# Performance work log

Measured on AMD Instinct MI355X. Metric: run time of the kernel, lower is better.

Reference implementation:

```python
import jax, jax.numpy as jnp
import numpy as np

L, H, NH, F, S_MAX, VOCAB, STAR_V, OFF = 12, 768, 12, 3072, 512, 31090, 390, 30700
EPS = 1e-12

def _ln(x, g, b):
    m = x.mean(-1, keepdims=True)
    v = ((x - m) ** 2).mean(-1, keepdims=True)
    return (x - m) * jax.lax.rsqrt(v + EPS) * g + b

def setup_inputs() -> dict:
    key = jax.random.key(0)
    ks = iter(jax.random.split(key, 48))
    B, S = 16, 512
    p = lambda *s: jax.random.normal(next(ks), s, dtype=jnp.float32) * 0.02
    return dict(
        input_ids=jax.random.randint(next(ks), (B, S), 0, VOCAB),
        attention_mask=jnp.ones((B, S), dtype=jnp.int32),
        token_type_ids=jnp.zeros((B, S), dtype=jnp.int32),
        word_emb=p(VOCAB, H), star_emb=p(STAR_V, H),
        pos_emb=p(S_MAX, H), type_emb=p(2, H),
        emb_g=jnp.ones(H), emb_b=jnp.zeros(H),
        Wq=p(L, H, H), bq=jnp.zeros((L, H)), Wk=p(L, H, H), bk=jnp.zeros((L, H)),
        Wv=p(L, H, H), bv=jnp.zeros((L, H)), Wo=p(L, H, H), bo=jnp.zeros((L, H)),
        g1=jnp.ones((L, H)), b1=jnp.zeros((L, H)),
        Wi=p(L, H, F), bi=jnp.zeros((L, F)), Wf=p(L, F, H), bf=jnp.zeros((L, H)),
        g2=jnp.ones((L, H)), b2=jnp.zeros((L, H)),
        pool_W=p(H, H), pool_b=jnp.zeros(H))

def reference(input_ids, attention_mask, token_type_ids, word_emb, star_emb,
              pos_emb, type_emb, emb_g, emb_b, Wq, bq, Wk, bk, Wv, bv, Wo, bo,
              g1, b1, Wi, bi, Wf, bf, g2, b2, pool_W, pool_b):
    B, S = input_ids.shape
    dh = H // NH
    # vectorized masked embedding swap (replaces the per-token Python loop)
    star = input_ids >= OFF
    embs = jnp.where(star[..., None],
                     star_emb[jnp.clip(input_ids - OFF, 0, STAR_V - 1)],
                     word_emb[jnp.clip(input_ids, 0, VOCAB - 1)])
    x = _ln(embs + pos_emb[:S][None] + type_emb[token_type_ids], emb_g, emb_b)
    ext = (1.0 - attention_mask.astype(x.dtype))[:, None, None, :] * -10000.0
    scale = 1.0 / np.sqrt(dh).astype(np.float32)

    def layer(x, pr):
        wq, bq_, wk, bk_, wv, bv_, wo, bo_, g1_, b1_, wi, bi_, wf, bf_, g2_, b2_ = pr
        sp = lambda t: t.reshape(B, S, NH, dh).transpose(0, 2, 1, 3)  # [B,NH,S,dh]
        q, k, v = sp(x @ wq + bq_), sp(x @ wk + bk_), sp(x @ wv + bv_)
        att = jax.nn.softmax(jnp.einsum('bhqd,bhkd->bhqk', q, k) * scale + ext, axis=-1)
        ctx = jnp.einsum('bhqk,bhkd->bhqd', att, v).transpose(0, 2, 1, 3).reshape(B, S, H)
        x = _ln(x + ctx @ wo + bo_, g1_, b1_)
        x = _ln(x + jax.nn.gelu(x @ wi + bi_, approximate=False) @ wf + bf_, g2_, b2_)
        return x, None

    x, _ = jax.lax.scan(layer, x, (Wq, bq, Wk, bk, Wv, bv, Wo, bo,
                                   g1, b1, Wi, bi, Wf, bf, g2, b2))
    pooled = jnp.tanh(x[:, 0] @ pool_W + pool_b)
    return x, pooled
```

## Files before the change

### kernel.cpp

```cpp
#include <hip/hip_runtime.h>
#include <hip/hip_bf16.h>
#include <math.h>


#define L_   12
#define H_   768
#define NH_  12
#define DH_  64
#define F_   3072
#define B_   16
#define S_   512
#define NTOK (B_ * S_)
#define QKVN 2304

typedef __attribute__((ext_vector_type(8))) __bf16 bf16x8;
typedef __attribute__((ext_vector_type(4))) __bf16 bf16x4;
typedef __attribute__((ext_vector_type(4))) float  f32x4;

static __device__ __forceinline__ f32x4 mfma16(bf16x8 a, bf16x8 b, f32x4 c) {
  return __builtin_amdgcn_mfma_f32_16x16x32_bf16(a, b, c, 0, 0, 0);
}

static __device__ __forceinline__ void load_lds16(const void* g, void* l) {
  __builtin_amdgcn_global_load_lds(
      (const __attribute__((address_space(1))) void*)g,
      (__attribute__((address_space(3))) void*)l, 16, 0, 0);
}

static __device__ __forceinline__ float gelu_fast(float v) {
  const float u = 1.5957691216057308f * v * (1.0f + 0.044715f * v * v);
  return v / (1.0f + __expf(-u));
}

__global__ __launch_bounds__(256) void transpose_k(const float* __restrict__ in,
                                                   __bf16* __restrict__ out,
                                                   int R, int C, size_t outZ) {
  __shared__ float t[32][33];
  const int z = blockIdx.z;
  const float* inz = in + (size_t)z * R * C;
  __bf16* outz = out + (size_t)z * outZ;
  const int c0 = blockIdx.x * 32, r0 = blockIdx.y * 32;
  const int tx = threadIdx.x, ty = threadIdx.y;
#pragma unroll
  for (int i = 0; i < 32; i += 8)
    t[ty + i][tx] = inz[(size_t)(r0 + ty + i) * C + c0 + tx];
  __syncthreads();
#pragma unroll
  for (int i = 0; i < 32; i += 8)
    outz[(size_t)(c0 + ty + i) * R + r0 + tx] = (__bf16)t[tx][ty + i];
}

__global__ __launch_bounds__(256) void concat_bias(const float* __restrict__ bq,
                                                   const float* __restrict__ bk,
                                                   const float* __restrict__ bv,
                                                   float* __restrict__ o) {
  const int i = blockIdx.x * 256 + threadIdx.x;
  if (i >= L_ * QKVN) return;
  const int l = i / QKVN, j = i - l * QKVN;
  float v;
  if (j < H_) v = bq[l * H_ + j];
  else if (j < 2 * H_) v = bk[l * H_ + j - H_];
  else v = bv[l * H_ + j - 2 * H_];
  o[i] = v;
}

template <int EPI, int OUTBF, int VT>
__global__ __launch_bounds__(256, 3) void gemm_n64(const __bf16* __restrict__ A,
                                                   const __bf16* __restrict__ Bt,
                                                   const float* __restrict__ bias,
                                                   float* __restrict__ Cf,
                                                   __bf16* __restrict__ Cb,
                                                   __bf16* __restrict__ vtp,
                                                   int M, int N, int K, int Ntiles) {
  alignas(16) __shared__ __bf16 lds[24576];
  const int tid = threadIdx.x, wid = tid >> 6, lane = tid & 63;
  int bid = blockIdx.x;
  const int nwg = gridDim.x;
  if ((nwg & 7) == 0) bid = (bid & 7) * (nwg >> 3) + (bid >> 3);
  const int bm = (bid / Ntiles) << 7, bn = (bid % Ntiles) << 6;
  const int nt = K >> 6;

  const __bf16* pA[4];
  const __bf16* pB[2];
#pragma unroll
  for (int j = 0; j < 4; ++j) {
    const int E = (j << 11) + tid * 8;
    const int Ep = E ^ (((E >> 8) & 1) << 4);
    const int r = ((Ep >> 10) << 4) | ((Ep >> 5) & 15);
    const int c = (((Ep >> 9) & 1) << 5) | (Ep & 31);
    pA[j] = A + (size_t)(bm + r) * K + c;
    if (j < 2) pB[j] = Bt + (size_t)(bn + r) * K + c;
  }

  auto stage = [&](int t, int buf) {
    __bf16* base = &lds[buf * 12288 + (wid << 9)];
    const size_t off = (size_t)(t << 6);
#pragma unroll
    for (int j = 0; j < 4; ++j) load_lds16(pA[j] + off, base + (j << 11));
#pragma unroll
    for (int j = 0; j < 2; ++j) load_lds16(pB[j] + off, base + 8192 + (j << 11));
  };

  const int frow = lane & 15, fk = (lane >> 4) << 3;
  const int swzb = (frow * 32 + fk) ^ (((frow >> 3) & 1) << 4);
  const int mh = wid >> 1, nq = wid & 1;

  f32x4 acc[4][2] = {};

  stage(0, 0);
  asm volatile("s_waitcnt vmcnt(0)" ::: "memory");
  __builtin_amdgcn_s_barrier();

  for (int t = 0; t < nt; ++t) {
    const int buf = t & 1;
    if (t + 1 < nt) stage(t + 1, buf ^ 1);
    const __bf16* LA = &lds[buf * 12288 + (mh << 12)];
    const __bf16* LB = &lds[buf * 12288 + 8192 + (nq << 11)];
    bf16x8 a[4][2], b[2][2];
#pragma unroll
    for (int mi = 0; mi < 4; ++mi)
#pragma unroll
      for (int ks = 0; ks < 2; ++ks)
        a[mi][ks] = *(const bf16x8*)&LA[mi * 1024 + ks * 512 + swzb];
#pragma unroll
    for (int ni = 0; ni < 2; ++ni)
#pragma unroll
      for (int ks = 0; ks < 2; ++ks)
        b[ni][ks] = *(const bf16x8*)&LB[ni * 1024 + ks * 512 + swzb];
    asm volatile("s_waitcnt lgkmcnt(0)" ::: "memory");
    __builtin_amdgcn_s_setprio(1);
#pragma unroll
    for (int mi = 0; mi < 4; ++mi)
#pragma unroll
      for (int ni = 0; ni < 2; ++ni)
#pragma unroll
        for (int ks = 0; ks < 2; ++ks)
          acc[mi][ni] = mfma16(a[mi][ks], b[ni][ks], acc[mi][ni]);
    __builtin_amdgcn_s_setprio(0);
    asm volatile("s_waitcnt vmcnt(0)" ::: "memory");
    __builtin_amdgcn_s_barrier();
  }

  const int r0 = (lane >> 4) << 2, c0 = lane & 15;
  const int wrow = bm + (mh << 6), wcol = bn + (nq << 5);
#pragma unroll
  for (int ni = 0; ni < 2; ++ni) {
    const int col = wcol + (ni << 4) + c0;
    const float bv = bias[col];
    if (VT && (wcol + (ni << 4)) >= 2 * H_) {
      const int hh = (col - 2 * H_) >> 6, dd = (col - 2 * H_) & 63;
#pragma unroll
      for (int mi = 0; mi < 4; ++mi) {
        const int row = wrow + (mi << 4) + r0;
        bf16x4 pv;
#pragma unroll
        for (int r = 0; r < 4; ++r) pv[r] = (__bf16)(acc[mi][ni][r] + bv);
        const int bb2 = row >> 9, ss = row & 511;
        *(bf16x4*)&vtp[((size_t)(bb2 * NH_ + hh) * DH_ + dd) * S_ + ss] = pv;
      }
    } else {
#pragma unroll
      for (int mi = 0; mi < 4; ++mi) {
        const int row = wrow + (mi << 4) + r0;
#pragma unroll
        for (int r = 0; r < 4; ++r) {
          float v = acc[mi][ni][r] + bv;
          if (EPI == 1) v = gelu_fast(v);
          if (OUTBF)
            Cb[(size_t)(row + r) * N + col] = (__bf16)v;
          else
            Cf[(size_t)(row + r) * N + col] = v;
        }
      }
    }
  }
}

__global__ __launch_bounds__(256, 3) void attn_kernel(const __bf16* __restrict__ qkv,
                                                      const __bf16* __restrict__ vt,
                                                      const int* __restrict__ amask,
                                                      __bf16* __restrict__ ctx) {
  __shared__ float extm[S_];
  alignas(16) __shared__ __bf16 Kl[2][2048];
  alignas(16) __shared__ __bf16 Vl[2][2048];
  __shared__ __bf16 Pl[4][2][16][40];
  const int h = blockIdx.x, b = blockIdx.y, z = blockIdx.z;
  const int tid = threadIdx.x, wid = tid >> 6, lane = tid & 63;
  const size_t rowb = (size_t)b * S_ * QKVN + (size_t)h * DH_;
  const __bf16* vbase = vt + ((size_t)(b * NH_ + h) * DH_) * S_;

  for (int i = tid; i < S_; i += 256)
    extm[i] = (1.0f - (float)amask[b * S_ + i]) * -10000.0f;

  const int E = tid * 8;
  const int Ep = E ^ (((E >> 8) & 1) << 4);
  const int krow = ((Ep >> 10) << 4) | ((Ep >> 5) & 15);
  const int kcol = (((Ep >> 9) & 1) << 5) | (Ep & 31);
  const __bf16* ksrc = qkv + rowb + (size_t)krow * QKVN + H_ + kcol;
  const int vd = ((Ep >> 9) << 4) | ((Ep >> 5) & 15);
  const int vs = Ep & 31;
  const __bf16* vsrc = vbase + (size_t)vd * S_ + vs;

  auto stageKV = [&](int kt, int buf) {
    load_lds16(ksrc + (size_t)(kt * 32) * QKVN, &Kl[buf][E]);
    load_lds16(vsrc + kt * 32, &Vl[buf][E]);
  };

  const int c0 = lane & 15, g4 = lane >> 4;
  const int swzb = (c0 * 32 + (g4 << 3)) ^ (((c0 >> 3) & 1) << 4);
  const int qt0 = z * 8 + wid * 2;
  bf16x8 qf[2][2];
#pragma unroll
  for (int qi = 0; qi < 2; ++qi) {
    const __bf16* qrow = qkv + rowb +
        (size_t)((qt0 + qi) * 16 + c0) * QKVN + (g4 << 3);
    qf[qi][0] = *(const bf16x8*)qrow;
    qf[qi][1] = *(const bf16x8*)(qrow + 32);
  }
  f32x4 oacc[2][4] = {};
  float mrow[2] = {-1e30f, -1e30f}, lsum[2] = {0.f, 0.f};

  stageKV(0, 0);
  asm volatile("s_waitcnt vmcnt(0)" ::: "memory");
  __syncthreads();

#pragma unroll
  for (int kt = 0; kt < 16; ++kt) {
    const int buf = kt & 1;
    if (kt + 1 < 16) stageKV(kt + 1, buf ^ 1);
    bf16x8 kf[2][2], vf[4];
#pragma unroll
    for (int f = 0; f < 2; ++f)
#pragma unroll
      for (int half = 0; half < 2; ++half)
        kf[f][half] = *(const bf16x8*)&Kl[buf][f * 1024 + half * 512 + swzb];
#pragma unroll
    for (int dt = 0; dt < 4; ++dt)
      vf[dt] = *(const bf16x8*)&Vl[buf][dt * 512 + swzb];
    asm volatile("s_waitcnt lgkmcnt(0)" ::: "memory");
#pragma unroll
    for (int qi = 0; qi < 2; ++qi) {
      f32x4 sc[2];
      __builtin_amdgcn_s_setprio(1);
#pragma unroll
      for (int f = 0; f < 2; ++f) {
        f32x4 z2 = {};
        z2 = mfma16(kf[f][0], qf[qi][0], z2);
        z2 = mfma16(kf[f][1], qf[qi][1], z2);
#pragma unroll
        for (int r = 0; r < 4; ++r)
          sc[f][r] = z2[r] * 0.125f + extm[kt * 32 + f * 16 + (g4 << 2) + r];
      }
      __builtin_amdgcn_s_setprio(0);
      float mx = fmaxf(fmaxf(fmaxf(sc[0][0], sc[0][1]), fmaxf(sc[0][2], sc[0][3])),
                       fmaxf(fmaxf(sc[1][0], sc[1][1]), fmaxf(sc[1][2], sc[1][3])));
      mx = fmaxf(mx, __shfl_xor(mx, 16, 64));
      mx = fmaxf(mx, __shfl_xor(mx, 32, 64));
      const float mn = fmaxf(mrow[qi], mx);
      const float al = __expf(mrow[qi] - mn);
      mrow[qi] = mn;
      float rs = 0.f;
      bf16x4 p0, p1;
#pragma unroll
      for (int r = 0; r < 4; ++r) {
        const float pa0 = __expf(sc[0][r] - mn);
        const float pa1 = __expf(sc[1][r] - mn);
        p0[r] = (__bf16)pa0;
        p1[r] = (__bf16)pa1;
        rs += pa0 + pa1;
      }
      rs += __shfl_xor(rs, 16, 64);
      rs += __shfl_xor(rs, 32, 64);
      lsum[qi] = lsum[qi] * al + rs;
      *(bf16x4*)&Pl[wid][qi][c0][(g4 << 2)] = p0;
      *(bf16x4*)&Pl[wid][qi][c0][16 + (g4 << 2)] = p1;
      float alr[4];
#pragma unroll
      for (int r = 0; r < 4; ++r)
        alr[r] = __shfl(al, (lane & 48) | ((g4 << 2) + r), 64);
#pragma unroll
      for (int dt = 0; dt < 4; ++dt)
#pragma unroll
        for (int r = 0; r < 4; ++r) oacc[qi][dt][r] *= alr[r];
      const bf16x8 pa = *(const bf16x8*)&Pl[wid][qi][c0][g4 << 3];
      __builtin_amdgcn_s_setprio(1);
#pragma unroll
      for (int dt = 0; dt < 4; ++dt)
        oacc[qi][dt] = mfma16(pa, vf[dt], oacc[qi][dt]);
      __builtin_amdgcn_s_setprio(0);
    }
    asm volatile("s_waitcnt vmcnt(0)" ::: "memory");
    __builtin_amdgcn_s_barrier();
  }
#pragma unroll
  for (int qi = 0; qi < 2; ++qi) {
    float inv[4];
#pragma unroll
    for (int r = 0; r < 4; ++r)
      inv[r] = 1.0f / __shfl(lsum[qi], (lane & 48) | ((g4 << 2) + r), 64);
#pragma unroll
    for (int dt = 0; dt < 4; ++dt)
#pragma unroll
      for (int r = 0; r < 4; ++r)
        ctx[(size_t)b * S_ * H_ + (size_t)h * DH_ +
            (size_t)((qt0 + qi) * 16 + (g4 << 2) + r) * H_ + dt * 16 + c0] =
            (__bf16)(oacc[qi][dt][r] * inv[r]);
  }
}

__global__ __launch_bounds__(256) void addln_kernel(float* __restrict__ x,
                                                    const __bf16* __restrict__ t,
                                                    const float* __restrict__ g,
                                                    const float* __restrict__ bb,
                                                    __bf16* __restrict__ xb) {
  const int tok = blockIdx.x * 4 + (threadIdx.x >> 6);
  const int lane = threadIdx.x & 63;
  float* xr = x + (size_t)tok * H_;
  const __bf16* tr = t + (size_t)tok * H_;
  f32x4 v[3];
  float s = 0.f, s2 = 0.f;
#pragma unroll
  for (int i = 0; i < 3; ++i) {
    const int off = lane * 4 + i * 256;
    f32x4 a = *(const f32x4*)&xr[off];
    bf16x4 tb = *(const bf16x4*)&tr[off];
#pragma unroll
    for (int r = 0; r < 4; ++r) {
      v[i][r] = a[r] + (float)tb[r];
      s += v[i][r];
      s2 += v[i][r] * v[i][r];
    }
  }
#pragma unroll
  for (int o = 32; o > 0; o >>= 1) {
    s += __shfl_xor(s, o, 64);
    s2 += __shfl_xor(s2, o, 64);
  }
  const float mean = s * (1.0f / 768.0f);
  const float var = s2 * (1.0f / 768.0f) - mean * mean;
  const float rstd = rsqrtf(var + 1e-12f);
  __bf16* xbr = xb + (size_t)tok * H_;
#pragma unroll
  for (int i = 0; i < 3; ++i) {
    const int off = lane * 4 + i * 256;
    f32x4 gv = *(const f32x4*)&g[off];
    f32x4 bv = *(const f32x4*)&bb[off];
    f32x4 y;
    bf16x4 yb;
#pragma unroll
    for (int r = 0; r < 4; ++r) {
      y[r] = (v[i][r] - mean) * rstd * gv[r] + bv[r];
      yb[r] = (__bf16)y[r];
    }
    *(f32x4*)&xr[off] = y;
    *(bf16x4*)&xbr[off] = yb;
  }
}

__global__ __launch_bounds__(256) void embed_kernel(
    const int* __restrict__ ids, const int* __restrict__ tt,
    const float* __restrict__ we, const float* __restrict__ se,
    const float* __restrict__ pe, const float* __restrict__ te,
    const float* __restrict__ g, const float* __restrict__ bb,
    float* __restrict__ x, __bf16* __restrict__ xb) {
  const int tok = blockIdx.x, tid = threadIdx.x;
  const int sp = tok & (S_ - 1);
  const int id = ids[tok];
  const float* e = (id >= 30700) ? se + (size_t)(id - 30700) * H_
                                 : we + (size_t)id * H_;
  const float* pr = pe + (size_t)sp * H_;
  const float* ty = te + (size_t)tt[tok] * H_;
  float v0 = e[tid] + pr[tid] + ty[tid];
  float v1 = e[tid + 256] + pr[tid + 256] + ty[tid + 256];
  float v2 = e[tid + 512] + pr[tid + 512] + ty[tid + 512];
  float s = v0 + v1 + v2;
  float s2 = v0 * v0 + v1 * v1 + v2 * v2;
  __shared__ float red1[4], red2[4];
#pragma unroll
  for (int o = 32; o > 0; o >>= 1) {
    s += __shfl_xor(s, o, 64);
    s2 += __shfl_xor(s2, o, 64);
  }
  if ((tid & 63) == 0) { red1[tid >> 6] = s; red2[tid >> 6] = s2; }
  __syncthreads();
  s = red1[0] + red1[1] + red1[2] + red1[3];
  s2 = red2[0] + red2[1] + red2[2] + red2[3];
  const float mean = s * (1.0f / 768.0f);
  const float var = s2 * (1.0f / 768.0f) - mean * mean;
  const float rstd = rsqrtf(var + 1e-12f);
  float* xr = x + (size_t)tok * H_;
  __bf16* xbr = xb + (size_t)tok * H_;
  const float y0 = (v0 - mean) * rstd * g[tid] + bb[tid];
  const float y1 = (v1 - mean) * rstd * g[tid + 256] + bb[tid + 256];
  const float y2 = (v2 - mean) * rstd * g[tid + 512] + bb[tid + 512];
  xr[tid] = y0; xr[tid + 256] = y1; xr[tid + 512] = y2;
  xbr[tid] = (__bf16)y0; xbr[tid + 256] = (__bf16)y1; xbr[tid + 512] = (__bf16)y2;
}

__global__ __launch_bounds__(256) void pool_kernel(const float* __restrict__ x,
                                                   const __bf16* __restrict__ wT,
                                                   const float* __restrict__ pb,
                                                   float* __restrict__ out) {
  const int b = blockIdx.x, tid = threadIdx.x;
  __shared__ float xr[H_];
  for (int i = tid; i < H_; i += 256) xr[i] = x[(size_t)b * S_ * H_ + i];
  __syncthreads();
  for (int n = tid; n < H_; n += 256) {
    const __bf16* w = wT + (size_t)n * H_;
    float acc = 0.f;
    for (int k = 0; k < H_; ++k) acc += xr[k] * (float)w[k];
    out[(size_t)b * H_ + n] = tanhf(acc + pb[n]);
  }
}

extern "C" void kernel_launch(void* const* d_in, const int* in_sizes, int n_in,
                              void* d_out, int out_size, void* d_ws,
                              size_t ws_size, hipStream_t stream) {
  (void)in_sizes; (void)n_in; (void)out_size;
  const int* ids = (const int*)d_in[0];
  const int* am = (const int*)d_in[1];
  const int* tt = (const int*)d_in[2];
  const float* we = (const float*)d_in[3];
  const float* se = (const float*)d_in[4];
  const float* pe = (const float*)d_in[5];
  const float* te = (const float*)d_in[6];
  const float* eg = (const float*)d_in[7];
  const float* ebb = (const float*)d_in[8];
  const float* Wq = (const float*)d_in[9];
  const float* bq = (const float*)d_in[10];
  const float* Wk = (const float*)d_in[11];
  const float* bk = (const float*)d_in[12];
  const float* Wv = (const float*)d_in[13];
  const float* bv = (const float*)d_in[14];
  const float* Wo = (const float*)d_in[15];
  const float* bo = (const float*)d_in[16];
  const float* g1 = (const float*)d_in[17];
  const float* b1 = (const float*)d_in[18];
  const float* Wi = (const float*)d_in[19];
  const float* bi = (const float*)d_in[20];
  const float* Wf = (const float*)d_in[21];
  const float* bf_ = (const float*)d_in[22];
  const float* g2 = (const float*)d_in[23];
  const float* b2 = (const float*)d_in[24];
  const float* pw = (const float*)d_in[25];
  const float* pb = (const float*)d_in[26];

  const size_t WQKV = (size_t)L_ * QKVN * H_;
  const size_t WSQ = (size_t)L_ * H_ * H_;
  const size_t WSF = (size_t)L_ * H_ * F_;
  const size_t MN = (size_t)NTOK * H_;
  __bf16* wqkv = (__bf16*)d_ws;
  __bf16* wTo_ = wqkv + WQKV;
  __bf16* wTi_ = wTo_ + WSQ;
  __bf16* wTf_ = wTi_ + WSF;
  __bf16* wTp_ = wTf_ + WSF;
  __bf16* xb = wTp_ + (size_t)H_ * H_;
  __bf16* qkvb = xb + MN;
  __bf16* cb = qkvb + (size_t)NTOK * QKVN;
  __bf16* mid = cb + MN;
  __bf16* vtb = mid + (size_t)NTOK * F_;
  __bf16* t0b = vtb + MN;
  float* bqkv = (float*)(t0b + MN);
  const size_t needed = (size_t)((char*)(bqkv + (size_t)L_ * QKVN) - (char*)d_ws);
  if (ws_size < needed) return;

  float* x = (float*)d_out;
  float* pooled = x + MN;

  const dim3 tb(32, 8);
  const size_t zq = (size_t)QKVN * H_;
  transpose_k<<<dim3(24, 24, 12), tb, 0, stream>>>(Wq, wqkv, H_, H_, zq);
  transpose_k<<<dim3(24, 24, 12), tb, 0, stream>>>(Wk, wqkv + (size_t)H_ * H_, H_, H_, zq);
  transpose_k<<<dim3(24, 24, 12), tb, 0, stream>>>(Wv, wqkv + 2 * (size_t)H_ * H_, H_, H_, zq);
  transpose_k<<<dim3(24, 24, 12), tb, 0, stream>>>(Wo, wTo_, H_, H_, (size_t)H_ * H_);
  transpose_k<<<dim3(96, 24, 12), tb, 0, stream>>>(Wi, wTi_, H_, F_, (size_t)H_ * F_);
  transpose_k<<<dim3(24, 96, 12), tb, 0, stream>>>(Wf, wTf_, F_, H_, (size_t)H_ * F_);
  transpose_k<<<dim3(24, 24, 1), tb, 0, stream>>>(pw, wTp_, H_, H_, (size_t)H_ * H_);
  concat_bias<<<(L_ * QKVN + 255) / 256, 256, 0, stream>>>(bq, bk, bv, bqkv);

  embed_kernel<<<NTOK, 256, 0, stream>>>(ids, tt, we, se, pe, te, eg, ebb, x, xb);

  for (int l = 0; l < L_; ++l) {
    gemm_n64<0, 1, 1><<<(NTOK / 128) * (QKVN / 64), 256, 0, stream>>>(
        xb, wqkv + (size_t)l * QKVN * H_, bqkv + (size_t)l * QKVN,
        nullptr, qkvb, vtb, NTOK, QKVN, H_, QKVN / 64);

    attn_kernel<<<dim3(NH_, B_, 4), 256, 0, stream>>>(qkvb, vtb, am, cb);

    gemm_n64<0, 1, 0><<<(NTOK / 128) * (H_ / 64), 256, 0, stream>>>(
        cb, wTo_ + (size_t)l * H_ * H_, bo + l * H_, nullptr, t0b, nullptr,
        NTOK, H_, H_, H_ / 64);
    addln_kernel<<<NTOK / 4, 256, 0, stream>>>(x, t0b, g1 + l * H_, b1 + l * H_, xb);

    gemm_n64<1, 1, 0><<<(NTOK / 128) * (F_ / 64), 256, 0, stream>>>(
        xb, wTi_ + (size_t)l * H_ * F_, bi + l * F_, nullptr, mid, nullptr,
        NTOK, F_, H_, F_ / 64);
    gemm_n64<0, 1, 0><<<(NTOK / 128) * (H_ / 64), 256, 0, stream>>>(
        mid, wTf_ + (size_t)l * F_ * H_, bf_ + l * H_, nullptr, t0b, nullptr,
        NTOK, H_, F_, H_ / 64);
    addln_kernel<<<NTOK / 4, 256, 0, stream>>>(x, t0b, g2 + l * H_, b2 + l * H_, xb);
  }

  pool_kernel<<<B_, 256, 0, stream>>>(x, wTp_, pb, pooled);
}
```

Before: 3.036 ms.

## Split attention work so each wave owns one query tile, doubling grid

The attention kernel now gives each wave a single 16-row query tile instead of two, and the grid's z dimension doubles from 4 to 8 so all 512 queries are still covered. Register pressure and per-block LDS drop, and the launch bound is raised to 6 blocks per SM to allow more concurrent waves. The trade-off is that each K/V tile staged into LDS is reused by half as many queries, so global K/V traffic doubles.

```diff
diff --git a/kernel.cpp b/kernel.cpp
--- a/kernel.cpp
+++ b/kernel.cpp
@@ -176,14 +176,14 @@
   }
 }
 
-__global__ __launch_bounds__(256, 3) void attn_kernel(const __bf16* __restrict__ qkv,
+__global__ __launch_bounds__(256, 6) void attn_kernel(const __bf16* __restrict__ qkv,
                                                       const __bf16* __restrict__ vt,
                                                       const int* __restrict__ amask,
                                                       __bf16* __restrict__ ctx) {
   __shared__ float extm[S_];
   alignas(16) __shared__ __bf16 Kl[2][2048];
   alignas(16) __shared__ __bf16 Vl[2][2048];
-  __shared__ __bf16 Pl[4][2][16][40];
+  __shared__ __bf16 Pl[4][16][40];
   const int h = blockIdx.x, b = blockIdx.y, z = blockIdx.z;
   const int tid = threadIdx.x, wid = tid >> 6, lane = tid & 63;
   const size_t rowb = (size_t)b * S_ * QKVN + (size_t)h * DH_;
@@ -208,17 +208,15 @@
 
   const int c0 = lane & 15, g4 = lane >> 4;
   const int swzb = (c0 * 32 + (g4 << 3)) ^ (((c0 >> 3) & 1) << 4);
-  const int qt0 = z * 8 + wid * 2;
-  bf16x8 qf[2][2];
-#pragma unroll
-  for (int qi = 0; qi < 2; ++qi) {
-    const __bf16* qrow = qkv + rowb +
-        (size_t)((qt0 + qi) * 16 + c0) * QKVN + (g4 << 3);
-    qf[qi][0] = *(const bf16x8*)qrow;
-    qf[qi][1] = *(const bf16x8*)(qrow + 32);
-  }
-  f32x4 oacc[2][4] = {};
-  float mrow[2] = {-1e30f, -1e30f}, lsum[2] = {0.f, 0.f};
+  const int qt = z * 4 + wid;
+  bf16x8 qf0, qf1;
+  {
+    const __bf16* qrow = qkv + rowb + (size_t)(qt * 16 + c0) * QKVN + (g4 << 3);
+    qf0 = *(const bf16x8*)qrow;
+    qf1 = *(const bf16x8*)(qrow + 32);
+  }
+  f32x4 oacc[4] = {};
+  float mrow = -1e30f, lsum = 0.f;
 
   stageKV(0, 0);
   asm volatile("s_waitcnt vmcnt(0)" ::: "memory");
@@ -238,74 +236,68 @@
     for (int dt = 0; dt < 4; ++dt)
       vf[dt] = *(const bf16x8*)&Vl[buf][dt * 512 + swzb];
     asm volatile("s_waitcnt lgkmcnt(0)" ::: "memory");
-#pragma unroll
-    for (int qi = 0; qi < 2; ++qi) {
-      f32x4 sc[2];
-      __builtin_amdgcn_s_setprio(1);
-#pragma unroll
-      for (int f = 0; f < 2; ++f) {
-        f32x4 z2 = {};
-        z2 = mfma16(kf[f][0], qf[qi][0], z2);
-        z2 = mfma16(kf[f][1], qf[qi][1], z2);
-#pragma unroll
-        for (int r = 0; r < 4; ++r)
-          sc[f][r] = z2[r] * 0.125f + extm[kt * 32 + f * 16 + (g4 << 2) + r];
-      }
-      __builtin_amdgcn_s_setprio(0);
-      float mx = fmaxf(fmaxf(fmaxf(sc[0][0], sc[0][1]), fmaxf(sc[0][2], sc[0][3])),
-                       fmaxf(fmaxf(sc[1][0], sc[1][1]), fmaxf(sc[1][2], sc[1][3])));
-      mx = fmaxf(mx, __shfl_xor(mx, 16, 64));
-      mx = fmaxf(mx, __shfl_xor(mx, 32, 64));
-      const float mn = fmaxf(mrow[qi], mx);
-      const float al = __expf(mrow[qi] - mn);
-      mrow[qi] = mn;
-      float rs = 0.f;
-      bf16x4 p0, p1;
-#pragma unroll
-      for (int r = 0; r < 4; ++r) {
-        const float pa0 = __expf(sc[0][r] - mn);
-        const float pa1 = __expf(sc[1][r] - mn);
-        p0[r] = (__bf16)pa0;
-        p1[r] = (__bf16)pa1;
-        rs += pa0 + pa1;
-      }
-      rs += __shfl_xor(rs, 16, 64);
-      rs += __shfl_xor(rs, 32, 64);
-      lsum[qi] = lsum[qi] * al + rs;
-      *(bf16x4*)&Pl[wid][qi][c0][(g4 << 2)] = p0;
-      *(bf16x4*)&Pl[wid][qi][c0][16 + (g4 << 2)] = p1;
-      float alr[4];
+    f32x4 sc[2];
+    __builtin_amdgcn_s_setprio(1);
+#pragma unroll
+    for (int f = 0; f < 2; ++f) {
+      f32x4 z2 = {};
+      z2 = mfma16(kf[f][0], qf0, z2);
+      z2 = mfma16(kf[f][1], qf1, z2);
 #pragma unroll
       for (int r = 0; r < 4; ++r)
-        alr[r] = __shfl(al, (lane & 48) | ((g4 << 2) + r), 64);
-#pragma unroll
-      for (int dt = 0; dt < 4; ++dt)
-#pragma unroll
-        for (int r = 0; r < 4; ++r) oacc[qi][dt][r] *= alr[r];
-      const bf16x8 pa = *(const bf16x8*)&Pl[wid][qi][c0][g4 << 3];
-      __builtin_amdgcn_s_setprio(1);
-#pragma unroll
-      for (int dt = 0; dt < 4; ++dt)
-        oacc[qi][dt] = mfma16(pa, vf[dt], oacc[qi][dt]);
-      __builtin_amdgcn_s_setprio(0);
+        sc[f][r] = z2[r] * 0.125f + extm[kt * 32 + f * 16 + (g4 << 2) + r];
     }
+    __builtin_amdgcn_s_setprio(0);
+    float mx = fmaxf(fmaxf(fmaxf(sc[0][0], sc[0][1]), fmaxf(sc[0][2], sc[0][3])),
+                     fmaxf(fmaxf(sc[1][0], sc[1][1]), fmaxf(sc[1][2], sc[1][3])));
+    mx = fmaxf(mx, __shfl_xor(mx, 16, 64));
+    mx = fmaxf(mx, __shfl_xor(mx, 32, 64));
+    const float mn = fmaxf(mrow, mx);
+    const float al = __expf(mrow - mn);
+    mrow = mn;
+    float rs = 0.f;
+    bf16x4 p0, p1;
+#pragma unroll
+    for (int r = 0; r < 4; ++r) {
+      const float pa0 = __expf(sc[0][r] - mn);
+      const float pa1 = __expf(sc[1][r] - mn);
+      p0[r] = (__bf16)pa0;
+      p1[r] = (__bf16)pa1;
+      rs += pa0 + pa1;
+    }
+    rs += __shfl_xor(rs, 16, 64);
+    rs += __shfl_xor(rs, 32, 64);
+    lsum = lsum * al + rs;
+    *(bf16x4*)&Pl[wid][c0][(g4 << 2)] = p0;
+    *(bf16x4*)&Pl[wid][c0][16 + (g4 << 2)] = p1;
+    float alr[4];
+#pragma unroll
+    for (int r = 0; r < 4; ++r)
+      alr[r] = __shfl(al, (lane & 48) | ((g4 << 2) + r), 64);
+#pragma unroll
+    for (int dt = 0; dt < 4; ++dt)
+#pragma unroll
+      for (int r = 0; r < 4; ++r) oacc[dt][r] *= alr[r];
+    const bf16x8 pa = *(const bf16x8*)&Pl[wid][c0][g4 << 3];
+    __builtin_amdgcn_s_setprio(1);
+#pragma unroll
+    for (int dt = 0; dt < 4; ++dt)
+      oacc[dt] = mfma16(pa, vf[dt], oacc[dt]);
+    __builtin_amdgcn_s_setprio(0);
     asm volatile("s_waitcnt vmcnt(0)" ::: "memory");
     __builtin_amdgcn_s_barrier();
   }
-#pragma unroll
-  for (int qi = 0; qi < 2; ++qi) {
-    float inv[4];
+  float inv[4];
+#pragma unroll
+  for (int r = 0; r < 4; ++r)
+    inv[r] = 1.0f / __shfl(lsum, (lane & 48) | ((g4 << 2) + r), 64);
+#pragma unroll
+  for (int dt = 0; dt < 4; ++dt)
 #pragma unroll
     for (int r = 0; r < 4; ++r)
-      inv[r] = 1.0f / __shfl(lsum[qi], (lane & 48) | ((g4 << 2) + r), 64);
-#pragma unroll
-    for (int dt = 0; dt < 4; ++dt)
-#pragma unroll
-      for (int r = 0; r < 4; ++r)
-        ctx[(size_t)b * S_ * H_ + (size_t)h * DH_ +
-            (size_t)((qt0 + qi) * 16 + (g4 << 2) + r) * H_ + dt * 16 + c0] =
-            (__bf16)(oacc[qi][dt][r] * inv[r]);
-  }
+      ctx[(size_t)b * S_ * H_ + (size_t)h * DH_ +
+          (size_t)(qt * 16 + (g4 << 2) + r) * H_ + dt * 16 + c0] =
+          (__bf16)(oacc[dt][r] * inv[r]);
 }
 
 __global__ __launch_bounds__(256) void addln_kernel(float* __restrict__ x,
@@ -485,7 +477,7 @@
         xb, wqkv + (size_t)l * QKVN * H_, bqkv + (size_t)l * QKVN,
         nullptr, qkvb, vtb, NTOK, QKVN, H_, QKVN / 64);
 
-    attn_kernel<<<dim3(NH_, B_, 4), 256, 0, stream>>>(qkvb, vtb, am, cb);
+    attn_kernel<<<dim3(NH_, B_, 8), 256, 0, stream>>>(qkvb, vtb, am, cb);
 
     gemm_n64<0, 1, 0><<<(NTOK / 128) * (H_ / 64), 256, 0, stream>>>(
         cb, wTo_ + (size_t)l * H_ * H_, bo + l * H_, nullptr, t0b, nullptr,
```

New measurement: 3.097 ms. 1.02x slower.
